# Kernel tuning notes

Measured on AMD Instinct MI355X. Metric: run time of the kernel, lower is better.

## Reference

```python
import jax, jax.numpy as jnp
import numpy as np

NHEAD = 8
MAX_RADIUS = 16
NEG_INF = float('-inf')


def setup_inputs() -> dict:
    key = jax.random.key(0)
    ks = jax.random.split(key, 6)
    B, T, D = 4, 2048, 512
    s = 1.0 / np.sqrt(D)
    return {
        'x': jax.random.normal(ks[0], (B, T, D), dtype=jnp.float32),
        'radius': jax.random.normal(ks[1], (NHEAD,), dtype=jnp.float32),
        'in_proj_weight': jax.random.normal(ks[2], (3 * D, D), dtype=jnp.float32) * s,
        'in_proj_bias': jax.random.normal(ks[3], (3 * D,), dtype=jnp.float32) * 0.02,
        'out_proj_weight': jax.random.normal(ks[4], (D, D), dtype=jnp.float32) * s,
        'out_proj_bias': jax.random.normal(ks[5], (D,), dtype=jnp.float32) * 0.02,
    }


def reference(x, radius, in_proj_weight, in_proj_bias, out_proj_weight, out_proj_bias):
    B, T, D = x.shape
    H = NHEAD
    hd = D // H
    scale = 1.0 / jnp.sqrt(jnp.asarray(hd, dtype=x.dtype))

    # fused QKV projection: [B,T,3D]
    qkv = x @ in_proj_weight.T + in_proj_bias
    q, k, v = jnp.split(qkv, 3, axis=-1)
    q = q.reshape(B, T, H, hd)
    k = k.reshape(B, T, H, hd)
    v = v.reshape(B, T, H, hd)

    # scores [B,H,T,T]
    scores = jnp.einsum('bqhd,bkhd->bhqk', q, k) * scale

    # per-head learned radius band mask
    r = jnp.clip(jax.nn.sigmoid(radius) * MAX_RADIUS, 1.0)  # [H]
    idx = jnp.arange(T)
    rel = jnp.abs(idx[None, :] - idx[:, None]).astype(x.dtype)  # [T,T]
    band = rel[None, :, :] <= r[:, None, None]  # [H,T,T]
    scores = jnp.where(band[None], scores, NEG_INF)

    attn = jax.nn.softmax(scores, axis=-1)
    out = jnp.einsum('bhqk,bkhd->bqhd', attn, v).reshape(B, T, D)
    return out @ out_proj_weight.T + out_proj_bias
```

## Files before the change

kernel.cpp:

```cpp
#include <hip/hip_runtime.h>
#include <hip/hip_bf16.h>
#include <cstdint>

#define T_LEN 2048
#define B_SZ 4
#define D_MOD 512
#define N_HEAD 8
#define HDIM 64
#define QKV_N 1536
#define M_ROWS 8192

typedef uint32_t u32;
typedef uint16_t u16;
typedef __attribute__((ext_vector_type(8))) __bf16 bf16x8;
typedef __attribute__((ext_vector_type(4))) float f32x4;

__device__ __forceinline__ u16 f2bf(float f) {
    u32 u = __builtin_bit_cast(u32, f);
    u32 r = (u + 0x7FFFu + ((u >> 16) & 1u)) >> 16;
    return (u16)r;
}
__device__ __forceinline__ float bf2f(u16 h) {
    u32 u = ((u32)h) << 16;
    return __builtin_bit_cast(float, u);
}

__global__ void cast3_kernel(const float* __restrict__ a, int na,
                             const float* __restrict__ b, int nb,
                             const float* __restrict__ c,
                             u16* __restrict__ oa, u16* __restrict__ ob, u16* __restrict__ oc) {
    int i8 = (blockIdx.x * blockDim.x + threadIdx.x) * 8;
    const float* src; u16* dst; int off;
    if (i8 < na)           { src = a; dst = oa; off = i8; }
    else if (i8 < na + nb) { src = b; dst = ob; off = i8 - na; }
    else                   { src = c; dst = oc; off = i8 - na - nb; }
    const float4* p = (const float4*)(src + off);
    float4 x = p[0], y = p[1];
    u32 r0 = (u32)f2bf(x.x) | ((u32)f2bf(x.y) << 16);
    u32 r1 = (u32)f2bf(x.z) | ((u32)f2bf(x.w) << 16);
    u32 r2 = (u32)f2bf(y.x) | ((u32)f2bf(y.y) << 16);
    u32 r3 = (u32)f2bf(y.z) | ((u32)f2bf(y.w) << 16);
    *(uint4*)(dst + off) = make_uint4(r0, r1, r2, r3);
}

#define BK 64

template <bool OUT_BF16, int BMt>
__global__ __launch_bounds__(256, 2)
void gemm_bt(const u16* __restrict__ A, const u16* __restrict__ B,
             const float* __restrict__ bias, void* __restrict__ C,
             int M, int N, int K)
{
    constexpr int WM = BMt / 2;
    constexpr int MI = WM / 16;
    __shared__ alignas(16) u16 lda[BMt * BK];
    __shared__ alignas(16) u16 ldb[128 * BK];
    const int tid  = threadIdx.x;
    const int wave = tid >> 6;
    const int lane = tid & 63;
    const int bn = blockIdx.x, bm = blockIdx.y;
    const int wm = wave >> 1, wn = wave & 1;

    f32x4 acc[MI][4] = {};

    const int srow8 = lane >> 3;
    const int sg    = (lane & 7) ^ srow8;
    const long a_base = (long)bm * BMt;
    const long b_base = (long)bn * 128;

    const int fr = lane & 15;
    const int fq = lane >> 4;
    int a_off[MI], b_off[4];
#pragma unroll
    for (int i = 0; i < MI; ++i) {
        int ra = wm * WM + i * 16 + fr;
        a_off[i] = ra * BK + ((fq ^ (ra & 7)) * 8);
    }
#pragma unroll
    for (int i = 0; i < 4; ++i) {
        int rb = wn * 64 + i * 16 + fr;
        b_off[i] = rb * BK + ((fq ^ (rb & 7)) * 8);
    }

    for (int kk = 0; kk < K; kk += BK) {
#pragma unroll
        for (int j = 0; j < BMt / 32; ++j) {
            int r = wave * (BMt / 4) + j * 8 + srow8;
            const u16* ga = A + (a_base + r) * (long)K + kk + sg * 8;
            __builtin_amdgcn_global_load_lds(
                (const __attribute__((address_space(1))) void*)ga,
                (__attribute__((address_space(3))) void*)&lda[(wave * (BMt / 4) + j * 8) * BK],
                16, 0, 0);
        }
#pragma unroll
        for (int j = 0; j < 4; ++j) {
            int r = wave * 32 + j * 8 + srow8;
            const u16* gb = B + (b_base + r) * (long)K + kk + sg * 8;
            __builtin_amdgcn_global_load_lds(
                (const __attribute__((address_space(1))) void*)gb,
                (__attribute__((address_space(3))) void*)&ldb[(wave * 32 + j * 8) * BK],
                16, 0, 0);
        }
        __syncthreads();
#pragma unroll
        for (int kh = 0; kh < 2; ++kh) {
            bf16x8 af[MI], bfr[4];
#pragma unroll
            for (int i = 0; i < MI; ++i) af[i]  = *(const bf16x8*)&lda[a_off[i] ^ (kh << 5)];
#pragma unroll
            for (int i = 0; i < 4; ++i) bfr[i] = *(const bf16x8*)&ldb[b_off[i] ^ (kh << 5)];
#pragma unroll
            for (int mi = 0; mi < MI; ++mi)
#pragma unroll
                for (int ni = 0; ni < 4; ++ni)
                    acc[mi][ni] = __builtin_amdgcn_mfma_f32_16x16x32_bf16(
                        af[mi], bfr[ni], acc[mi][ni], 0, 0, 0);
        }
        __syncthreads();
    }

    const long row0 = a_base + wm * WM;
    const long col0 = b_base + wn * 64;
#pragma unroll
    for (int mi = 0; mi < MI; ++mi) {
#pragma unroll
        for (int ni = 0; ni < 4; ++ni) {
            long col = col0 + ni * 16 + fr;
            float bv = bias[col];
            long rowb = row0 + mi * 16 + fq * 4;
#pragma unroll
            for (int rr = 0; rr < 4; ++rr) {
                float v = acc[mi][ni][rr] + bv;
                long idx = (rowb + rr) * (long)N + col;
                if (OUT_BF16) ((u16*)C)[idx] = f2bf(v);
                else          ((float*)C)[idx] = v;
            }
        }
    }
}

#define AQ 128
#define AW 16
#define AROWS (AQ + 2 * AW)
#define ASTR 70

__device__ __forceinline__ void unpack16(const u32* __restrict__ src, float* __restrict__ dst) {
#pragma unroll
    for (int dd = 0; dd < 8; ++dd) {
        u32 wv = src[dd];
        dst[2 * dd]     = bf2f((u16)(wv & 0xffffu));
        dst[2 * dd + 1] = bf2f((u16)(wv >> 16));
    }
}

__global__ __launch_bounds__(256)
void attn_kernel(const u16* __restrict__ qkv, const float* __restrict__ radius,
                 u16* __restrict__ out)
{
    __shared__ u16 ks[AROWS * ASTR];
    __shared__ u16 vs[AROWS * ASTR];

    const int tid = threadIdx.x;
    const int bid = blockIdx.x;
    const int qc = bid & 15;
    const int h  = (bid >> 4) & 7;
    const int b  = bid >> 7;
    const int q0 = qc * AQ;

    float rad = radius[h];
    float r = 16.0f / (1.0f + __expf(-rad));
    r = fmaxf(r, 1.0f);
    const int w = (int)floorf(r);

    for (int cid = tid; cid < AROWS * 4; cid += 256) {
        int row = cid >> 2;
        int ch  = cid & 3;
        int t = min(max(q0 - AW + row, 0), T_LEN - 1);
        const u16* gk = qkv + ((long)(b * T_LEN + t)) * QKV_N + D_MOD + h * HDIM + ch * 16;
        const u16* gv = gk + D_MOD;
        uint4 k0 = *(const uint4*)gk, k1 = *(const uint4*)(gk + 8);
        uint4 v0 = *(const uint4*)gv, v1 = *(const uint4*)(gv + 8);
        u32* kd = (u32*)&ks[row * ASTR + ch * 18];
        u32* vd = (u32*)&vs[row * ASTR + ch * 18];
        kd[0] = k0.x; kd[1] = k0.y; kd[2] = k0.z; kd[3] = k0.w;
        kd[4] = k1.x; kd[5] = k1.y; kd[6] = k1.z; kd[7] = k1.w;
        vd[0] = v0.x; vd[1] = v0.y; vd[2] = v0.z; vd[3] = v0.w;
        vd[4] = v1.x; vd[5] = v1.y; vd[6] = v1.z; vd[7] = v1.w;
    }

    const int p = tid >> 2;
    const int g = tid & 3;
    const int qA = q0 + 2 * p;
    const long rowA = (long)(b * T_LEN + qA);
    const long rowB = rowA + 1;

    float qregA[16], qregB[16];
    {
        const u16* gq = qkv + rowA * QKV_N + h * HDIM + g * 16;
        u32 wa[8], wb[8];
        uint4 t0 = *(const uint4*)gq,              t1 = *(const uint4*)(gq + 8);
        uint4 t2 = *(const uint4*)(gq + QKV_N),    t3 = *(const uint4*)(gq + QKV_N + 8);
        wa[0]=t0.x; wa[1]=t0.y; wa[2]=t0.z; wa[3]=t0.w; wa[4]=t1.x; wa[5]=t1.y; wa[6]=t1.z; wa[7]=t1.w;
        wb[0]=t2.x; wb[1]=t2.y; wb[2]=t2.z; wb[3]=t2.w; wb[4]=t3.x; wb[5]=t3.y; wb[6]=t3.z; wb[7]=t3.w;
#pragma unroll
        for (int j = 0; j < 8; ++j) {
            qregA[2 * j]     = bf2f((u16)(wa[j] & 0xffffu)) * 0.125f;
            qregA[2 * j + 1] = bf2f((u16)(wa[j] >> 16))     * 0.125f;
            qregB[2 * j]     = bf2f((u16)(wb[j] & 0xffffu)) * 0.125f;
            qregB[2 * j + 1] = bf2f((u16)(wb[j] >> 16))     * 0.125f;
        }
    }
    __syncthreads();

    float mA = -1e30f, lA = 0.0f, mB = -1e30f, lB = 0.0f;
    float accA[16], accB[16];
#pragma unroll
    for (int d = 0; d < 16; ++d) { accA[d] = 0.0f; accB[d] = 0.0f; }

    const int imax = 2 * w + 1;
    for (int i = 0; i <= imax; ++i) {
        int jrow = 2 * p - w + i;
        int j = q0 + jrow;
        int row = jrow + AW;
        float kf[16];
        unpack16((const u32*)&ks[row * ASTR + g * 18], kf);
        float sA = 0.0f, sB = 0.0f;
#pragma unroll
        for (int d = 0; d < 16; ++d) { sA += qregA[d] * kf[d]; sB += qregB[d] * kf[d]; }
        sA += __shfl_xor(sA, 1); sA += __shfl_xor(sA, 2);
        sB += __shfl_xor(sB, 1); sB += __shfl_xor(sB, 2);
        bool inb = ((unsigned)j) < (unsigned)T_LEN;
        bool vA = inb && (i < imax);
        bool vB = inb && (i > 0);
        float mnA = fmaxf(mA, vA ? sA : -1e30f);
        float scA = __expf(mA - mnA);
        float pA  = vA ? __expf(sA - mnA) : 0.0f;
        mA = mnA; lA = lA * scA + pA;
        float mnB = fmaxf(mB, vB ? sB : -1e30f);
        float scB = __expf(mB - mnB);
        float pB  = vB ? __expf(sB - mnB) : 0.0f;
        mB = mnB; lB = lB * scB + pB;
        float vf[16];
        unpack16((const u32*)&vs[row * ASTR + g * 18], vf);
#pragma unroll
        for (int d = 0; d < 16; ++d) {
            accA[d] = accA[d] * scA + pA * vf[d];
            accB[d] = accB[d] * scB + pB * vf[d];
        }
    }

    float invA = 1.0f / lA;
    float invB = 1.0f / lB;
    u32 oA[8], oB[8];
#pragma unroll
    for (int j2 = 0; j2 < 8; ++j2) {
        oA[j2] = (u32)f2bf(accA[2 * j2] * invA) | ((u32)f2bf(accA[2 * j2 + 1] * invA) << 16);
        oB[j2] = (u32)f2bf(accB[2 * j2] * invB) | ((u32)f2bf(accB[2 * j2 + 1] * invB) << 16);
    }
    u16* poA = out + rowA * D_MOD + h * HDIM + g * 16;
    u16* poB = out + rowB * D_MOD + h * HDIM + g * 16;
    *(uint4*)poA       = make_uint4(oA[0], oA[1], oA[2], oA[3]);
    *(uint4*)(poA + 8) = make_uint4(oA[4], oA[5], oA[6], oA[7]);
    *(uint4*)poB       = make_uint4(oB[0], oB[1], oB[2], oB[3]);
    *(uint4*)(poB + 8) = make_uint4(oB[4], oB[5], oB[6], oB[7]);
}

extern "C" void kernel_launch(void* const* d_in, const int* in_sizes, int n_in,
                              void* d_out, int out_size, void* d_ws, size_t ws_size,
                              hipStream_t stream)
{
    (void)in_sizes; (void)n_in; (void)out_size; (void)ws_size;
    const float* x      = (const float*)d_in[0];
    const float* radius = (const float*)d_in[1];
    const float* w_in   = (const float*)d_in[2];
    const float* b_in   = (const float*)d_in[3];
    const float* w_out  = (const float*)d_in[4];
    const float* b_out  = (const float*)d_in[5];
    float* outp = (float*)d_out;

    char* ws = (char*)d_ws;
    u16* x_bf    = (u16*)ws;  ws += (size_t)M_ROWS * D_MOD * 2;
    u16* win_bf  = (u16*)ws;  ws += (size_t)QKV_N * D_MOD * 2;
    u16* wout_bf = (u16*)ws;  ws += (size_t)D_MOD * D_MOD * 2;
    u16* qkv_bf  = (u16*)ws;  ws += (size_t)M_ROWS * QKV_N * 2;
    u16* attn_bf = (u16*)ws;

    const int na = M_ROWS * D_MOD;
    const int nb = QKV_N * D_MOD;
    const int nc = D_MOD * D_MOD;
    cast3_kernel<<<(na + nb + nc) / 2048, 256, 0, stream>>>(
        x, na, w_in, nb, w_out, x_bf, win_bf, wout_bf);

    gemm_bt<true, 128><<<dim3(QKV_N / 128, M_ROWS / 128), 256, 0, stream>>>(
        x_bf, win_bf, b_in, qkv_bf, M_ROWS, QKV_N, D_MOD);
    attn_kernel<<<B_SZ * N_HEAD * (T_LEN / AQ), 256, 0, stream>>>(qkv_bf, radius, attn_bf);
    gemm_bt<false, 64><<<dim3(D_MOD / 128, M_ROWS / 64), 256, 0, stream>>>(
        attn_bf, wout_bf, b_out, outp, M_ROWS, D_MOD, D_MOD);
}
```

Measured before the change: 128.2 us.

## Fuse cast, QKV GEMM, attention and output GEMM into one persistent kernel

```diff
diff --git a/kernel.cpp b/kernel.cpp
--- a/kernel.cpp
+++ b/kernel.cpp
@@ -9,6 +9,7 @@
 #define HDIM 64
 #define QKV_N 1536
 #define M_ROWS 8192
+#define GRID_BLKS 512
 
 typedef uint32_t u32;
 typedef uint16_t u16;
@@ -25,40 +26,34 @@
     return __builtin_bit_cast(float, u);
 }
 
-__global__ void cast3_kernel(const float* __restrict__ a, int na,
-                             const float* __restrict__ b, int nb,
-                             const float* __restrict__ c,
-                             u16* __restrict__ oa, u16* __restrict__ ob, u16* __restrict__ oc) {
-    int i8 = (blockIdx.x * blockDim.x + threadIdx.x) * 8;
-    const float* src; u16* dst; int off;
-    if (i8 < na)           { src = a; dst = oa; off = i8; }
-    else if (i8 < na + nb) { src = b; dst = ob; off = i8 - na; }
-    else                   { src = c; dst = oc; off = i8 - na - nb; }
-    const float4* p = (const float4*)(src + off);
-    float4 x = p[0], y = p[1];
-    u32 r0 = (u32)f2bf(x.x) | ((u32)f2bf(x.y) << 16);
-    u32 r1 = (u32)f2bf(x.z) | ((u32)f2bf(x.w) << 16);
-    u32 r2 = (u32)f2bf(y.x) | ((u32)f2bf(y.y) << 16);
-    u32 r3 = (u32)f2bf(y.z) | ((u32)f2bf(y.w) << 16);
-    *(uint4*)(dst + off) = make_uint4(r0, r1, r2, r3);
+__global__ void init_bar(u32* bar) {
+    if (threadIdx.x < 16) bar[threadIdx.x] = 0u;
+}
+
+__device__ __forceinline__ void grid_barrier(u32* cnt, u32 target) {
+    __syncthreads();
+    if (threadIdx.x == 0) {
+        __threadfence();
+        atomicAdd(cnt, 1u);
+        while (atomicAdd(cnt, 0u) < target) __builtin_amdgcn_s_sleep(8);
+        __threadfence();
+    }
+    __syncthreads();
 }
 
 #define BK 64
 
 template <bool OUT_BF16, int BMt>
-__global__ __launch_bounds__(256, 2)
-void gemm_bt(const u16* __restrict__ A, const u16* __restrict__ B,
-             const float* __restrict__ bias, void* __restrict__ C,
-             int M, int N, int K)
+__device__ __forceinline__
+void gemm_tile(const u16* __restrict__ A, const u16* __restrict__ B,
+               const float* __restrict__ bias, void* __restrict__ C,
+               int M, int N, int K, int bm, int bn,
+               u16* lda, u16* ldb, int tid)
 {
     constexpr int WM = BMt / 2;
     constexpr int MI = WM / 16;
-    __shared__ alignas(16) u16 lda[BMt * BK];
-    __shared__ alignas(16) u16 ldb[128 * BK];
-    const int tid  = threadIdx.x;
     const int wave = tid >> 6;
     const int lane = tid & 63;
-    const int bn = blockIdx.x, bm = blockIdx.y;
     const int wm = wave >> 1, wn = wave & 1;
 
     f32x4 acc[MI][4] = {};
@@ -139,9 +134,9 @@
     }
 }
 
-#define AQ 128
+#define AQ 64
 #define AW 16
-#define AROWS (AQ + 2 * AW)
+#define AROWS 96
 #define ASTR 70
 
 __device__ __forceinline__ void unpack16(const u32* __restrict__ src, float* __restrict__ dst) {
@@ -153,23 +148,17 @@
     }
 }
 
-__global__ __launch_bounds__(256)
-void attn_kernel(const u16* __restrict__ qkv, const float* __restrict__ radius,
-                 u16* __restrict__ out)
+__device__ __forceinline__
+void attn_block64(const u16* __restrict__ qkv, const float* __restrict__ radius,
+                  u16* __restrict__ out, int id, int tid, u16* ks, u16* vs)
 {
-    __shared__ u16 ks[AROWS * ASTR];
-    __shared__ u16 vs[AROWS * ASTR];
-
-    const int tid = threadIdx.x;
-    const int bid = blockIdx.x;
-    const int qc = bid & 15;
-    const int h  = (bid >> 4) & 7;
-    const int b  = bid >> 7;
+    const int qc = id & 31;
+    const int h  = (id >> 5) & 7;
+    const int b  = id >> 8;
     const int q0 = qc * AQ;
 
     float rad = radius[h];
-    float r = 16.0f / (1.0f + __expf(-rad));
-    r = fmaxf(r, 1.0f);
+    float r = fmaxf(16.0f / (1.0f + __expf(-rad)), 1.0f);
     const int w = (int)floorf(r);
 
     for (int cid = tid; cid < AROWS * 4; cid += 256) {
@@ -188,81 +177,110 @@
         vd[4] = v1.x; vd[5] = v1.y; vd[6] = v1.z; vd[7] = v1.w;
     }
 
-    const int p = tid >> 2;
-    const int g = tid & 3;
-    const int qA = q0 + 2 * p;
-    const long rowA = (long)(b * T_LEN + qA);
-    const long rowB = rowA + 1;
-
-    float qregA[16], qregB[16];
+    const int qi = tid >> 2;
+    const int g  = tid & 3;
+    const int q  = q0 + qi;
+    const long rowq = (long)(b * T_LEN + q);
+
+    float qreg[16];
     {
-        const u16* gq = qkv + rowA * QKV_N + h * HDIM + g * 16;
-        u32 wa[8], wb[8];
-        uint4 t0 = *(const uint4*)gq,              t1 = *(const uint4*)(gq + 8);
-        uint4 t2 = *(const uint4*)(gq + QKV_N),    t3 = *(const uint4*)(gq + QKV_N + 8);
-        wa[0]=t0.x; wa[1]=t0.y; wa[2]=t0.z; wa[3]=t0.w; wa[4]=t1.x; wa[5]=t1.y; wa[6]=t1.z; wa[7]=t1.w;
-        wb[0]=t2.x; wb[1]=t2.y; wb[2]=t2.z; wb[3]=t2.w; wb[4]=t3.x; wb[5]=t3.y; wb[6]=t3.z; wb[7]=t3.w;
+        const u16* gq = qkv + rowq * QKV_N + h * HDIM + g * 16;
+        uint4 t0 = *(const uint4*)gq, t1 = *(const uint4*)(gq + 8);
+        u32 ww[8] = {t0.x, t0.y, t0.z, t0.w, t1.x, t1.y, t1.z, t1.w};
 #pragma unroll
         for (int j = 0; j < 8; ++j) {
-            qregA[2 * j]     = bf2f((u16)(wa[j] & 0xffffu)) * 0.125f;
-            qregA[2 * j + 1] = bf2f((u16)(wa[j] >> 16))     * 0.125f;
-            qregB[2 * j]     = bf2f((u16)(wb[j] & 0xffffu)) * 0.125f;
-            qregB[2 * j + 1] = bf2f((u16)(wb[j] >> 16))     * 0.125f;
+            qreg[2 * j]     = bf2f((u16)(ww[j] & 0xffffu)) * 0.125f;
+            qreg[2 * j + 1] = bf2f((u16)(ww[j] >> 16))     * 0.125f;
         }
     }
     __syncthreads();
 
-    float mA = -1e30f, lA = 0.0f, mB = -1e30f, lB = 0.0f;
-    float accA[16], accB[16];
-#pragma unroll
-    for (int d = 0; d < 16; ++d) { accA[d] = 0.0f; accB[d] = 0.0f; }
-
-    const int imax = 2 * w + 1;
-    for (int i = 0; i <= imax; ++i) {
-        int jrow = 2 * p - w + i;
-        int j = q0 + jrow;
-        int row = jrow + AW;
+    float m = -1e30f, l = 0.0f;
+    float acc[16];
+#pragma unroll
+    for (int d = 0; d < 16; ++d) acc[d] = 0.0f;
+
+    for (int rel = -w; rel <= w; ++rel) {
+        int j = q + rel;
+        if (((unsigned)j) >= (unsigned)T_LEN) continue;
+        int row = qi + AW + rel;
         float kf[16];
         unpack16((const u32*)&ks[row * ASTR + g * 18], kf);
-        float sA = 0.0f, sB = 0.0f;
-#pragma unroll
-        for (int d = 0; d < 16; ++d) { sA += qregA[d] * kf[d]; sB += qregB[d] * kf[d]; }
-        sA += __shfl_xor(sA, 1); sA += __shfl_xor(sA, 2);
-        sB += __shfl_xor(sB, 1); sB += __shfl_xor(sB, 2);
-        bool inb = ((unsigned)j) < (unsigned)T_LEN;
-        bool vA = inb && (i < imax);
-        bool vB = inb && (i > 0);
-        float mnA = fmaxf(mA, vA ? sA : -1e30f);
-        float scA = __expf(mA - mnA);
-        float pA  = vA ? __expf(sA - mnA) : 0.0f;
-        mA = mnA; lA = lA * scA + pA;
-        float mnB = fmaxf(mB, vB ? sB : -1e30f);
-        float scB = __expf(mB - mnB);
-        float pB  = vB ? __expf(sB - mnB) : 0.0f;
-        mB = mnB; lB = lB * scB + pB;
+        float s = 0.0f;
+#pragma unroll
+        for (int d = 0; d < 16; ++d) s += qreg[d] * kf[d];
+        s += __shfl_xor(s, 1);
+        s += __shfl_xor(s, 2);
+        float mn = fmaxf(m, s);
+        float sc = __expf(m - mn);
+        float p  = __expf(s - mn);
+        m = mn;
+        l = l * sc + p;
         float vf[16];
         unpack16((const u32*)&vs[row * ASTR + g * 18], vf);
 #pragma unroll
-        for (int d = 0; d < 16; ++d) {
-            accA[d] = accA[d] * scA + pA * vf[d];
-            accB[d] = accB[d] * scB + pB * vf[d];
-        }
-    }
-
-    float invA = 1.0f / lA;
-    float invB = 1.0f / lB;
-    u32 oA[8], oB[8];
-#pragma unroll
-    for (int j2 = 0; j2 < 8; ++j2) {
-        oA[j2] = (u32)f2bf(accA[2 * j2] * invA) | ((u32)f2bf(accA[2 * j2 + 1] * invA) << 16);
-        oB[j2] = (u32)f2bf(accB[2 * j2] * invB) | ((u32)f2bf(accB[2 * j2 + 1] * invB) << 16);
-    }
-    u16* poA = out + rowA * D_MOD + h * HDIM + g * 16;
-    u16* poB = out + rowB * D_MOD + h * HDIM + g * 16;
-    *(uint4*)poA       = make_uint4(oA[0], oA[1], oA[2], oA[3]);
-    *(uint4*)(poA + 8) = make_uint4(oA[4], oA[5], oA[6], oA[7]);
-    *(uint4*)poB       = make_uint4(oB[0], oB[1], oB[2], oB[3]);
-    *(uint4*)(poB + 8) = make_uint4(oB[4], oB[5], oB[6], oB[7]);
+        for (int d = 0; d < 16; ++d) acc[d] = acc[d] * sc + p * vf[d];
+    }
+
+    float inv = 1.0f / l;
+    u32 o[8];
+#pragma unroll
+    for (int j2 = 0; j2 < 8; ++j2)
+        o[j2] = (u32)f2bf(acc[2 * j2] * inv) | ((u32)f2bf(acc[2 * j2 + 1] * inv) << 16);
+    u16* po = out + rowq * D_MOD + h * HDIM + g * 16;
+    *(uint4*)po       = make_uint4(o[0], o[1], o[2], o[3]);
+    *(uint4*)(po + 8) = make_uint4(o[4], o[5], o[6], o[7]);
+}
+
+__global__ __launch_bounds__(256, 2)
+void fused_kernel(const float* __restrict__ x, const float* __restrict__ radius,
+                  const float* __restrict__ w_in, const float* __restrict__ b_in,
+                  const float* __restrict__ w_out, const float* __restrict__ b_out,
+                  float* __restrict__ out,
+                  u16* __restrict__ x_bf, u16* __restrict__ win_bf,
+                  u16* __restrict__ wout_bf, u16* __restrict__ qkv_bf,
+                  u16* __restrict__ attn_bf, u32* __restrict__ bar)
+{
+    __shared__ alignas(16) u16 smem[16384];
+    const int tid = threadIdx.x;
+    const int bid = blockIdx.x;
+
+    {
+        const int na = M_ROWS * D_MOD;
+        const int nb = QKV_N * D_MOD;
+        int c = bid * 256 + tid;
+#pragma unroll
+        for (int it = 0; it < 5; ++it, c += GRID_BLKS * 256) {
+            int i8 = c * 8;
+            const float* src; u16* dst; int off;
+            if (i8 < na)           { src = x;     dst = x_bf;    off = i8; }
+            else if (i8 < na + nb) { src = w_in;  dst = win_bf;  off = i8 - na; }
+            else                   { src = w_out; dst = wout_bf; off = i8 - na - nb; }
+            const float4* pp = (const float4*)(src + off);
+            float4 a = pp[0], bq = pp[1];
+            u32 r0 = (u32)f2bf(a.x) | ((u32)f2bf(a.y) << 16);
+            u32 r1 = (u32)f2bf(a.z) | ((u32)f2bf(a.w) << 16);
+            u32 r2 = (u32)f2bf(bq.x) | ((u32)f2bf(bq.y) << 16);
+            u32 r3 = (u32)f2bf(bq.z) | ((u32)f2bf(bq.w) << 16);
+            *(uint4*)(dst + off) = make_uint4(r0, r1, r2, r3);
+        }
+    }
+    grid_barrier(bar + 0, GRID_BLKS);
+
+    for (int t = bid; t < 768; t += GRID_BLKS)
+        gemm_tile<true, 128>(x_bf, win_bf, b_in, qkv_bf,
+                             M_ROWS, QKV_N, D_MOD, t & 63, t >> 6,
+                             smem, smem + 128 * BK, tid);
+    grid_barrier(bar + 1, GRID_BLKS);
+
+    attn_block64(qkv_bf, radius, attn_bf, bid, tid, smem, smem + AROWS * ASTR);
+    __syncthreads();
+    attn_block64(qkv_bf, radius, attn_bf, bid + GRID_BLKS, tid, smem, smem + AROWS * ASTR);
+    grid_barrier(bar + 2, GRID_BLKS);
+
+    gemm_tile<false, 64>(attn_bf, wout_bf, b_out, out,
+                         M_ROWS, D_MOD, D_MOD, bid >> 2, bid & 3,
+                         smem, smem + 64 * BK, tid);
 }
 
 extern "C" void kernel_launch(void* const* d_in, const int* in_sizes, int n_in,
@@ -283,17 +301,11 @@
     u16* win_bf  = (u16*)ws;  ws += (size_t)QKV_N * D_MOD * 2;
     u16* wout_bf = (u16*)ws;  ws += (size_t)D_MOD * D_MOD * 2;
     u16* qkv_bf  = (u16*)ws;  ws += (size_t)M_ROWS * QKV_N * 2;
-    u16* attn_bf = (u16*)ws;
-
-    const int na = M_ROWS * D_MOD;
-    const int nb = QKV_N * D_MOD;
-    const int nc = D_MOD * D_MOD;
-    cast3_kernel<<<(na + nb + nc) / 2048, 256, 0, stream>>>(
-        x, na, w_in, nb, w_out, x_bf, win_bf, wout_bf);
-
-    gemm_bt<true, 128><<<dim3(QKV_N / 128, M_ROWS / 128), 256, 0, stream>>>(
-        x_bf, win_bf, b_in, qkv_bf, M_ROWS, QKV_N, D_MOD);
-    attn_kernel<<<B_SZ * N_HEAD * (T_LEN / AQ), 256, 0, stream>>>(qkv_bf, radius, attn_bf);
-    gemm_bt<false, 64><<<dim3(D_MOD / 128, M_ROWS / 64), 256, 0, stream>>>(
-        attn_bf, wout_bf, b_out, outp, M_ROWS, D_MOD, D_MOD);
-}
+    u16* attn_bf = (u16*)ws;  ws += (size_t)M_ROWS * D_MOD * 2;
+    u32* bar     = (u32*)ws;
+
+    init_bar<<<1, 64, 0, stream>>>(bar);
+    fused_kernel<<<GRID_BLKS, 256, 0, stream>>>(
+        x, radius, w_in, b_in, w_out, b_out, outp,
+        x_bf, win_bf, wout_bf, qkv_bf, attn_bf, bar);
+}
```

Measured after the change: 283.0 us. 121% more time.

## Fuse fp32-to-bf16 casts into GEMM tile loads, dropping separate cast kernel

Applied to the files above, without the earlier changes.

```diff
diff --git a/kernel.cpp b/kernel.cpp
--- a/kernel.cpp
+++ b/kernel.cpp
@@ -9,6 +9,7 @@
 #define HDIM 64
 #define QKV_N 1536
 #define M_ROWS 8192
+#define BK 64
 
 typedef uint32_t u32;
 typedef uint16_t u16;
@@ -25,116 +26,192 @@
     return __builtin_bit_cast(float, u);
 }
 
-__global__ void cast3_kernel(const float* __restrict__ a, int na,
-                             const float* __restrict__ b, int nb,
-                             const float* __restrict__ c,
-                             u16* __restrict__ oa, u16* __restrict__ ob, u16* __restrict__ oc) {
-    int i8 = (blockIdx.x * blockDim.x + threadIdx.x) * 8;
-    const float* src; u16* dst; int off;
-    if (i8 < na)           { src = a; dst = oa; off = i8; }
-    else if (i8 < na + nb) { src = b; dst = ob; off = i8 - na; }
-    else                   { src = c; dst = oc; off = i8 - na - nb; }
-    const float4* p = (const float4*)(src + off);
-    float4 x = p[0], y = p[1];
-    u32 r0 = (u32)f2bf(x.x) | ((u32)f2bf(x.y) << 16);
-    u32 r1 = (u32)f2bf(x.z) | ((u32)f2bf(x.w) << 16);
-    u32 r2 = (u32)f2bf(y.x) | ((u32)f2bf(y.y) << 16);
-    u32 r3 = (u32)f2bf(y.z) | ((u32)f2bf(y.w) << 16);
-    *(uint4*)(dst + off) = make_uint4(r0, r1, r2, r3);
-}
-
-#define BK 64
-
-template <bool OUT_BF16, int BMt>
+__device__ __forceinline__ bf16x8 pack8(float4 lo, float4 hi) {
+    union { u32 u[4]; bf16x8 v; } r;
+    r.u[0] = __builtin_amdgcn_perm(__builtin_bit_cast(u32, lo.y), __builtin_bit_cast(u32, lo.x), 0x07060302u);
+    r.u[1] = __builtin_amdgcn_perm(__builtin_bit_cast(u32, lo.w), __builtin_bit_cast(u32, lo.z), 0x07060302u);
+    r.u[2] = __builtin_amdgcn_perm(__builtin_bit_cast(u32, hi.y), __builtin_bit_cast(u32, hi.x), 0x07060302u);
+    r.u[3] = __builtin_amdgcn_perm(__builtin_bit_cast(u32, hi.w), __builtin_bit_cast(u32, hi.z), 0x07060302u);
+    return r.v;
+}
+
 __global__ __launch_bounds__(256, 2)
-void gemm_bt(const u16* __restrict__ A, const u16* __restrict__ B,
-             const float* __restrict__ bias, void* __restrict__ C,
-             int M, int N, int K)
+void gemm1_f32(const float* __restrict__ A, const float* __restrict__ B,
+               const float* __restrict__ bias, u16* __restrict__ C,
+               int M, int N, int K)
 {
-    constexpr int WM = BMt / 2;
-    constexpr int MI = WM / 16;
-    __shared__ alignas(16) u16 lda[BMt * BK];
-    __shared__ alignas(16) u16 ldb[128 * BK];
+    __shared__ alignas(16) float ldaf[128 * BK];
+    __shared__ alignas(16) float ldbf[128 * BK];
     const int tid  = threadIdx.x;
     const int wave = tid >> 6;
     const int lane = tid & 63;
     const int bn = blockIdx.x, bm = blockIdx.y;
     const int wm = wave >> 1, wn = wave & 1;
 
-    f32x4 acc[MI][4] = {};
-
-    const int srow8 = lane >> 3;
-    const int sg    = (lane & 7) ^ srow8;
-    const long a_base = (long)bm * BMt;
+    f32x4 acc[4][4] = {};
+
+    const int srow4 = lane >> 4;
+    const int slot  = lane & 15;
+    const long a_base = (long)bm * 128;
     const long b_base = (long)bn * 128;
-
     const int fr = lane & 15;
     const int fq = lane >> 4;
-    int a_off[MI], b_off[4];
-#pragma unroll
-    for (int i = 0; i < MI; ++i) {
-        int ra = wm * WM + i * 16 + fr;
-        a_off[i] = ra * BK + ((fq ^ (ra & 7)) * 8);
-    }
-#pragma unroll
-    for (int i = 0; i < 4; ++i) {
-        int rb = wn * 64 + i * 16 + fr;
-        b_off[i] = rb * BK + ((fq ^ (rb & 7)) * 8);
-    }
 
     for (int kk = 0; kk < K; kk += BK) {
 #pragma unroll
-        for (int j = 0; j < BMt / 32; ++j) {
-            int r = wave * (BMt / 4) + j * 8 + srow8;
-            const u16* ga = A + (a_base + r) * (long)K + kk + sg * 8;
+        for (int j = 0; j < 8; ++j) {
+            int rloc = j * 4 + srow4;
+            int gc = slot ^ (rloc & 15);
+            int r = wave * 32 + rloc;
+            const float* ga = A + (a_base + r) * (long)K + kk + gc * 4;
             __builtin_amdgcn_global_load_lds(
                 (const __attribute__((address_space(1))) void*)ga,
-                (__attribute__((address_space(3))) void*)&lda[(wave * (BMt / 4) + j * 8) * BK],
+                (__attribute__((address_space(3))) void*)&ldaf[(wave * 32 + j * 4) * BK],
                 16, 0, 0);
         }
 #pragma unroll
-        for (int j = 0; j < 4; ++j) {
-            int r = wave * 32 + j * 8 + srow8;
-            const u16* gb = B + (b_base + r) * (long)K + kk + sg * 8;
+        for (int j = 0; j < 8; ++j) {
+            int rloc = j * 4 + srow4;
+            int gc = slot ^ (rloc & 15);
+            int r = wave * 32 + rloc;
+            const float* gb = B + (b_base + r) * (long)K + kk + gc * 4;
             __builtin_amdgcn_global_load_lds(
                 (const __attribute__((address_space(1))) void*)gb,
-                (__attribute__((address_space(3))) void*)&ldb[(wave * 32 + j * 8) * BK],
+                (__attribute__((address_space(3))) void*)&ldbf[(wave * 32 + j * 4) * BK],
                 16, 0, 0);
         }
         __syncthreads();
 #pragma unroll
         for (int kh = 0; kh < 2; ++kh) {
-            bf16x8 af[MI], bfr[4];
-#pragma unroll
-            for (int i = 0; i < MI; ++i) af[i]  = *(const bf16x8*)&lda[a_off[i] ^ (kh << 5)];
-#pragma unroll
-            for (int i = 0; i < 4; ++i) bfr[i] = *(const bf16x8*)&ldb[b_off[i] ^ (kh << 5)];
-#pragma unroll
-            for (int mi = 0; mi < MI; ++mi)
+            bf16x8 af[4], bfr[4];
+#pragma unroll
+            for (int i = 0; i < 4; ++i) {
+                int ra = wm * 64 + i * 16 + fr;
+                int c0 = ((fq << 1) ^ (kh << 3)) ^ (ra & 15);
+                float4 lo = *(const float4*)&ldaf[ra * BK + c0 * 4];
+                float4 hi = *(const float4*)&ldaf[ra * BK + (c0 ^ 1) * 4];
+                af[i] = pack8(lo, hi);
+            }
+#pragma unroll
+            for (int i = 0; i < 4; ++i) {
+                int rb = wn * 64 + i * 16 + fr;
+                int c0 = ((fq << 1) ^ (kh << 3)) ^ (rb & 15);
+                float4 lo = *(const float4*)&ldbf[rb * BK + c0 * 4];
+                float4 hi = *(const float4*)&ldbf[rb * BK + (c0 ^ 1) * 4];
+                bfr[i] = pack8(lo, hi);
+            }
+#pragma unroll
+            for (int mi = 0; mi < 4; ++mi)
 #pragma unroll
                 for (int ni = 0; ni < 4; ++ni)
                     acc[mi][ni] = __builtin_amdgcn_mfma_f32_16x16x32_bf16(
-                        af[mi], bfr[ni], acc[mi][ni], 0, 0, 0);
+                        bfr[ni], af[mi], acc[mi][ni], 0, 0, 0);
         }
         __syncthreads();
     }
 
-    const long row0 = a_base + wm * WM;
+    const long row0 = a_base + wm * 64;
     const long col0 = b_base + wn * 64;
 #pragma unroll
-    for (int mi = 0; mi < MI; ++mi) {
+    for (int mi = 0; mi < 4; ++mi) {
+        long row = row0 + mi * 16 + fr;
 #pragma unroll
         for (int ni = 0; ni < 4; ++ni) {
-            long col = col0 + ni * 16 + fr;
-            float bv = bias[col];
-            long rowb = row0 + mi * 16 + fq * 4;
-#pragma unroll
-            for (int rr = 0; rr < 4; ++rr) {
-                float v = acc[mi][ni][rr] + bv;
-                long idx = (rowb + rr) * (long)N + col;
-                if (OUT_BF16) ((u16*)C)[idx] = f2bf(v);
-                else          ((float*)C)[idx] = v;
+            long col = col0 + ni * 16 + fq * 4;
+            float4 bv = *(const float4*)&bias[col];
+            u32 lo = (u32)f2bf(acc[mi][ni][0] + bv.x) | ((u32)f2bf(acc[mi][ni][1] + bv.y) << 16);
+            u32 hi = (u32)f2bf(acc[mi][ni][2] + bv.z) | ((u32)f2bf(acc[mi][ni][3] + bv.w) << 16);
+            *(uint2*)(C + row * (long)N + col) = make_uint2(lo, hi);
+        }
+    }
+}
+
+__global__ __launch_bounds__(256, 3)
+void gemm2_mix(const u16* __restrict__ A, const float* __restrict__ B,
+               const float* __restrict__ bias, float* __restrict__ C,
+               int M, int N, int K)
+{
+    __shared__ alignas(16) u16   lda16[64 * BK];
+    __shared__ alignas(16) float ldbf[128 * BK];
+    const int tid  = threadIdx.x;
+    const int wave = tid >> 6;
+    const int lane = tid & 63;
+    const int bn = blockIdx.x, bm = blockIdx.y;
+    const int wm = wave >> 1, wn = wave & 1;
+
+    f32x4 acc[2][4] = {};
+
+    const int srow8 = lane >> 3;
+    const int slot8 = lane & 7;
+    const int srow4 = lane >> 4;
+    const int slot16 = lane & 15;
+    const long a_base = (long)bm * 64;
+    const long b_base = (long)bn * 128;
+    const int fr = lane & 15;
+    const int fq = lane >> 4;
+
+    for (int kk = 0; kk < K; kk += BK) {
+#pragma unroll
+        for (int j = 0; j < 2; ++j) {
+            int rloc = j * 8 + srow8;
+            int gc = slot8 ^ (rloc & 7);
+            int r = wave * 16 + rloc;
+            const u16* ga = A + (a_base + r) * (long)K + kk + gc * 8;
+            __builtin_amdgcn_global_load_lds(
+                (const __attribute__((address_space(1))) void*)ga,
+                (__attribute__((address_space(3))) void*)&lda16[(wave * 16 + j * 8) * BK],
+                16, 0, 0);
+        }
+#pragma unroll
+        for (int j = 0; j < 8; ++j) {
+            int rloc = j * 4 + srow4;
+            int gc = slot16 ^ (rloc & 15);
+            int r = wave * 32 + rloc;
+            const float* gb = B + (b_base + r) * (long)K + kk + gc * 4;
+            __builtin_amdgcn_global_load_lds(
+                (const __attribute__((address_space(1))) void*)gb,
+                (__attribute__((address_space(3))) void*)&ldbf[(wave * 32 + j * 4) * BK],
+                16, 0, 0);
+        }
+        __syncthreads();
+#pragma unroll
+        for (int kh = 0; kh < 2; ++kh) {
+            bf16x8 af[2], bfr[4];
+#pragma unroll
+            for (int i = 0; i < 2; ++i) {
+                int ra = wm * 32 + i * 16 + fr;
+                af[i] = *(const bf16x8*)&lda16[(ra * BK + ((fq ^ (ra & 7)) * 8)) ^ (kh << 5)];
             }
+#pragma unroll
+            for (int i = 0; i < 4; ++i) {
+                int rb = wn * 64 + i * 16 + fr;
+                int c0 = ((fq << 1) ^ (kh << 3)) ^ (rb & 15);
+                float4 lo = *(const float4*)&ldbf[rb * BK + c0 * 4];
+                float4 hi = *(const float4*)&ldbf[rb * BK + (c0 ^ 1) * 4];
+                bfr[i] = pack8(lo, hi);
+            }
+#pragma unroll
+            for (int mi = 0; mi < 2; ++mi)
+#pragma unroll
+                for (int ni = 0; ni < 4; ++ni)
+                    acc[mi][ni] = __builtin_amdgcn_mfma_f32_16x16x32_bf16(
+                        bfr[ni], af[mi], acc[mi][ni], 0, 0, 0);
+        }
+        __syncthreads();
+    }
+
+    const long row0 = a_base + wm * 32;
+    const long col0 = b_base + wn * 64;
+#pragma unroll
+    for (int mi = 0; mi < 2; ++mi) {
+        long row = row0 + mi * 16 + fr;
+#pragma unroll
+        for (int ni = 0; ni < 4; ++ni) {
+            long col = col0 + ni * 16 + fq * 4;
+            float4 bv = *(const float4*)&bias[col];
+            *(float4*)(C + row * (long)N + col) = make_float4(
+                acc[mi][ni][0] + bv.x, acc[mi][ni][1] + bv.y,
+                acc[mi][ni][2] + bv.z, acc[mi][ni][3] + bv.w);
         }
     }
 }
@@ -168,8 +245,7 @@
     const int q0 = qc * AQ;
 
     float rad = radius[h];
-    float r = 16.0f / (1.0f + __expf(-rad));
-    r = fmaxf(r, 1.0f);
+    float r = fmaxf(16.0f / (1.0f + __expf(-rad)), 1.0f);
     const int w = (int)floorf(r);
 
     for (int cid = tid; cid < AROWS * 4; cid += 256) {
@@ -279,21 +355,12 @@
     float* outp = (float*)d_out;
 
     char* ws = (char*)d_ws;
-    u16* x_bf    = (u16*)ws;  ws += (size_t)M_ROWS * D_MOD * 2;
-    u16* win_bf  = (u16*)ws;  ws += (size_t)QKV_N * D_MOD * 2;
-    u16* wout_bf = (u16*)ws;  ws += (size_t)D_MOD * D_MOD * 2;
     u16* qkv_bf  = (u16*)ws;  ws += (size_t)M_ROWS * QKV_N * 2;
     u16* attn_bf = (u16*)ws;
 
-    const int na = M_ROWS * D_MOD;
-    const int nb = QKV_N * D_MOD;
-    const int nc = D_MOD * D_MOD;
-    cast3_kernel<<<(na + nb + nc) / 2048, 256, 0, stream>>>(
-        x, na, w_in, nb, w_out, x_bf, win_bf, wout_bf);
-
-    gemm_bt<true, 128><<<dim3(QKV_N / 128, M_ROWS / 128), 256, 0, stream>>>(
-        x_bf, win_bf, b_in, qkv_bf, M_ROWS, QKV_N, D_MOD);
+    gemm1_f32<<<dim3(QKV_N / 128, M_ROWS / 128), 256, 0, stream>>>(
+        x, w_in, b_in, qkv_bf, M_ROWS, QKV_N, D_MOD);
     attn_kernel<<<B_SZ * N_HEAD * (T_LEN / AQ), 256, 0, stream>>>(qkv_bf, radius, attn_bf);
-    gemm_bt<false, 64><<<dim3(D_MOD / 128, M_ROWS / 64), 256, 0, stream>>>(
-        attn_bf, wout_bf, b_out, outp, M_ROWS, D_MOD, D_MOD);
-}
+    gemm2_mix<<<dim3(D_MOD / 128, M_ROWS / 64), 256, 0, stream>>>(
+        attn_bf, w_out, b_out, outp, M_ROWS, D_MOD, D_MOD);
+}
```

Result: slower. 147.7 us (+15.2%).
